# Kernel tuning notes

Measured on AMD Instinct MI355X. Metric: run time of the kernel, lower is better.

The kernel has to match this reference:

```python
import jax, jax.numpy as jnp
import numpy as np

NUM_ENTS = 1000
NUM_RELS = 100
HIDDEN = 200
N_QUERY = 50000
N_HIST = 1000000
ALPHA = 0.5


def setup_inputs() -> dict:
    key = jax.random.key(0)
    ks = jax.random.split(key, 12)
    s = 0.05  # small init for numerical stability (xavier-like scale)
    return {
        "ent_emb": jax.random.normal(ks[0], (NUM_ENTS, HIDDEN), jnp.float32) * s,
        "rel_emb": jax.random.normal(ks[1], (NUM_RELS, HIDDEN), jnp.float32) * s,
        "tim_emb": jax.random.normal(ks[2], (1, HIDDEN), jnp.float32) * s,
        "g_w": jax.random.normal(ks[3], (3 * HIDDEN, HIDDEN), jnp.float32) * s,
        "g_b": jnp.zeros((HIDDEN,), jnp.float32),
        "c_w": jax.random.normal(ks[4], (3 * HIDDEN, HIDDEN), jnp.float32) * s,
        "c_b": jnp.zeros((HIDDEN,), jnp.float32),
        "hist_sub": jax.random.randint(ks[5], (N_HIST,), 0, NUM_ENTS, jnp.int32),
        "hist_rel": jax.random.randint(ks[6], (N_HIST,), 0, NUM_RELS, jnp.int32),
        "hist_obj": jax.random.randint(ks[7], (N_HIST,), 0, NUM_ENTS, jnp.int32),
        "sub": jax.random.randint(ks[8], (N_QUERY,), 0, NUM_ENTS, jnp.int32),
        "rel": jax.random.randint(ks[9], (N_QUERY,), 0, NUM_RELS, jnp.int32),
    }


def reference(ent_emb, rel_emb, tim_emb, g_w, g_b, c_w, c_b,
              hist_sub, hist_rel, hist_obj, sub, rel):
    E = ent_emb.shape[0]
    R = rel_emb.shape[0]
    N = sub.shape[0]
    # Triple-count histogram over all history graphs (fused scatter-add;
    # equivalent to the per-graph python loop vocab[s,r,o] += 1).
    vocab = jnp.zeros((E, R, E), jnp.float32).at[hist_sub, hist_rel, hist_obj].add(1.0)
    # Query features: [N, 3H]
    x = jnp.concatenate(
        [ent_emb[sub], rel_emb[rel], jnp.broadcast_to(tim_emb, (N, tim_emb.shape[1]))],
        axis=1)
    # Generate-mode score distribution
    gscore = jax.nn.softmax(x @ g_w + g_b, axis=1)  # [N, H]
    # Copy-mode mask: 1 where the (sub, rel) pair occurred in history
    mask = (vocab[sub, rel].sum(axis=1, keepdims=True) != 0).astype(x.dtype)  # [N, 1]
    cscore = jax.nn.softmax(jnp.tanh(x @ c_w + c_b) + mask, axis=1)  # [N, H]
    fscore = gscore + ALPHA * (cscore - gscore)
    return jnp.log(fscore)
```

## Files before the change

### kernel.cpp

```cpp
#include <hip/hip_runtime.h>
#include <math.h>

#define HIDDEN 200
#define ROWS_PER_BLOCK 4

__global__ __launch_bounds__(256) void precompute_kernel(
    const float* __restrict__ ent, const float* __restrict__ rel,
    const float* __restrict__ tim,
    const float* __restrict__ g_w, const float* __restrict__ g_b,
    const float* __restrict__ c_w, const float* __restrict__ c_b,
    float* __restrict__ Ag, float* __restrict__ Bg, float* __restrict__ Tg,
    float* __restrict__ Ac, float* __restrict__ Bc, float* __restrict__ Tc) {
  const float* in;
  const float* w;
  const float* bias = nullptr;
  float* out;
  int nrows, k0;
  switch (blockIdx.y) {
    case 0:  in = ent; w = g_w; out = Ag; nrows = 1000; k0 = 0;   break;
    case 1:  in = rel; w = g_w; out = Bg; nrows = 100;  k0 = 200; break;
    case 2:  in = tim; w = g_w; out = Tg; nrows = 1;    k0 = 400; bias = g_b; break;
    case 3:  in = ent; w = c_w; out = Ac; nrows = 1000; k0 = 0;   break;
    case 4:  in = rel; w = c_w; out = Bc; nrows = 100;  k0 = 200; break;
    default: in = tim; w = c_w; out = Tc; nrows = 1;    k0 = 400; bias = c_b; break;
  }
  int row0 = blockIdx.x * ROWS_PER_BLOCK;
  if (row0 >= nrows) return;
  int nr = nrows - row0;
  if (nr > ROWS_PER_BLOCK) nr = ROWS_PER_BLOCK;

  __shared__ float a_lds[ROWS_PER_BLOCK][HIDDEN];
  int c = threadIdx.x;
  if (c < HIDDEN) {
    for (int j = 0; j < nr; ++j) a_lds[j][c] = in[(row0 + j) * HIDDEN + c];
  }
  __syncthreads();
  if (c >= HIDDEN) return;

  float acc[ROWS_PER_BLOCK] = {0.f, 0.f, 0.f, 0.f};
  const float* wp = w + k0 * HIDDEN + c;
  #pragma unroll 4
  for (int k = 0; k < HIDDEN; ++k) {
    float wv = wp[k * HIDDEN];
    #pragma unroll
    for (int j = 0; j < ROWS_PER_BLOCK; ++j) acc[j] += a_lds[j][k] * wv;
  }
  float bv = bias ? bias[c] : 0.f;
  for (int j = 0; j < nr; ++j) out[(row0 + j) * HIDDEN + c] = acc[j] + bv;
}

__global__ __launch_bounds__(256) void query_kernel(
    const float* __restrict__ Ag, const float* __restrict__ Bg,
    const float* __restrict__ Tg, const float* __restrict__ Ac,
    const float* __restrict__ Bc, const float* __restrict__ Tc,
    const int* __restrict__ sub, const int* __restrict__ rel,
    float* __restrict__ out, int N) {
  int gtid = blockIdx.x * blockDim.x + threadIdx.x;
  int q = gtid >> 6;
  int lane = threadIdx.x & 63;
  if (q >= N) return;

  int s = sub[q];
  int r = rel[q];
  bool act = lane < (HIDDEN / 4);

  float lg[4], lc[4];
  float mg = -INFINITY, mc = -INFINITY;
  if (act) {
    float4 a = ((const float4*)(Ag + s * HIDDEN))[lane];
    float4 b = ((const float4*)(Bg + r * HIDDEN))[lane];
    float4 t = ((const float4*)Tg)[lane];
    lg[0] = a.x + b.x + t.x;
    lg[1] = a.y + b.y + t.y;
    lg[2] = a.z + b.z + t.z;
    lg[3] = a.w + b.w + t.w;
    a = ((const float4*)(Ac + s * HIDDEN))[lane];
    b = ((const float4*)(Bc + r * HIDDEN))[lane];
    t = ((const float4*)Tc)[lane];
    lc[0] = tanhf(a.x + b.x + t.x);
    lc[1] = tanhf(a.y + b.y + t.y);
    lc[2] = tanhf(a.z + b.z + t.z);
    lc[3] = tanhf(a.w + b.w + t.w);
    #pragma unroll
    for (int j = 0; j < 4; ++j) {
      mg = fmaxf(mg, lg[j]);
      mc = fmaxf(mc, lc[j]);
    }
  }
  #pragma unroll
  for (int m = 32; m > 0; m >>= 1) {
    mg = fmaxf(mg, __shfl_xor(mg, m));
    mc = fmaxf(mc, __shfl_xor(mc, m));
  }

  float eg[4], ec[4];
  float sg = 0.f, sc = 0.f;
  if (act) {
    #pragma unroll
    for (int j = 0; j < 4; ++j) {
      eg[j] = expf(lg[j] - mg);
      ec[j] = expf(lc[j] - mc);
      sg += eg[j];
      sc += ec[j];
    }
  }
  #pragma unroll
  for (int m = 32; m > 0; m >>= 1) {
    sg += __shfl_xor(sg, m);
    sc += __shfl_xor(sc, m);
  }

  if (act) {
    float ig = 0.5f / sg;
    float ic = 0.5f / sc;
    float4 o;
    o.x = logf(eg[0] * ig + ec[0] * ic);
    o.y = logf(eg[1] * ig + ec[1] * ic);
    o.z = logf(eg[2] * ig + ec[2] * ic);
    o.w = logf(eg[3] * ig + ec[3] * ic);
    ((float4*)(out + q * HIDDEN))[lane] = o;
  }
}

extern "C" void kernel_launch(void* const* d_in, const int* in_sizes, int n_in,
                              void* d_out, int out_size, void* d_ws, size_t ws_size,
                              hipStream_t stream) {
  const float* ent  = (const float*)d_in[0];
  const float* relE = (const float*)d_in[1];
  const float* tim  = (const float*)d_in[2];
  const float* g_w  = (const float*)d_in[3];
  const float* g_b  = (const float*)d_in[4];
  const float* c_w  = (const float*)d_in[5];
  const float* c_b  = (const float*)d_in[6];
  const int* sub = (const int*)d_in[10];
  const int* rel = (const int*)d_in[11];
  float* out = (float*)d_out;
  int N = in_sizes[10];

  float* ws = (float*)d_ws;
  float* Ag = ws;
  float* Ac = ws + 200000;
  float* Bg = ws + 400000;
  float* Bc = ws + 420000;
  float* Tg = ws + 440000;
  float* Tc = ws + 440200;

  dim3 grid1((1000 + ROWS_PER_BLOCK - 1) / ROWS_PER_BLOCK, 6);
  precompute_kernel<<<grid1, 256, 0, stream>>>(ent, relE, tim, g_w, g_b, c_w,
                                               c_b, Ag, Bg, Tg, Ac, Bc, Tc);

  long long threads = (long long)N * 64;
  int blocks = (int)((threads + 255) / 256);
  query_kernel<<<blocks, 256, 0, stream>>>(Ag, Bg, Tg, Ac, Bc, Tc, sub, rel,
                                           out, N);
}
```

Baseline: 131.5 us.

## Fold time term into relation tables, drop softmax max pass, use fast intrinsics

The precompute folds the time-embedding projection and bias into the relation tables, so the query kernel does two gathers per branch instead of three. The query kernel drops the max-reduction pass of both softmaxes, relying on small logits (tanh is bounded and the inputs are small), and uses hardware exp2/rcp/log intrinsics with a clamped exp-based tanh. It also broadcasts indices with readfirstlane, uses nontemporal output stores, and doubles rows per block in the precompute. The trade is numerical robustness: skipping max subtraction can overflow for large generate-mode logits, and the fast intrinsics are less accurate.

```diff
diff --git a/kernel.cpp b/kernel.cpp
--- a/kernel.cpp
+++ b/kernel.cpp
@@ -2,57 +2,73 @@
 #include <math.h>
 
 #define HIDDEN 200
-#define ROWS_PER_BLOCK 4
+#define RPB 8
+
+#define LOG2E 1.4426950408889634f
+#define LN2   0.6931471805599453f
+
+typedef float f32x4 __attribute__((ext_vector_type(4)));
 
 __global__ __launch_bounds__(256) void precompute_kernel(
     const float* __restrict__ ent, const float* __restrict__ rel,
     const float* __restrict__ tim,
     const float* __restrict__ g_w, const float* __restrict__ g_b,
     const float* __restrict__ c_w, const float* __restrict__ c_b,
-    float* __restrict__ Ag, float* __restrict__ Bg, float* __restrict__ Tg,
-    float* __restrict__ Ac, float* __restrict__ Bc, float* __restrict__ Tc) {
+    float* __restrict__ Ag, float* __restrict__ Ac,
+    float* __restrict__ Bg, float* __restrict__ Bc) {
   const float* in;
   const float* w;
   const float* bias = nullptr;
   float* out;
   int nrows, k0;
+  bool fold_tim = false;
   switch (blockIdx.y) {
     case 0:  in = ent; w = g_w; out = Ag; nrows = 1000; k0 = 0;   break;
-    case 1:  in = rel; w = g_w; out = Bg; nrows = 100;  k0 = 200; break;
-    case 2:  in = tim; w = g_w; out = Tg; nrows = 1;    k0 = 400; bias = g_b; break;
-    case 3:  in = ent; w = c_w; out = Ac; nrows = 1000; k0 = 0;   break;
-    case 4:  in = rel; w = c_w; out = Bc; nrows = 100;  k0 = 200; break;
-    default: in = tim; w = c_w; out = Tc; nrows = 1;    k0 = 400; bias = c_b; break;
+    case 1:  in = ent; w = c_w; out = Ac; nrows = 1000; k0 = 0;   break;
+    case 2:  in = rel; w = g_w; out = Bg; nrows = 100;  k0 = 200;
+             fold_tim = true; bias = g_b; break;
+    default: in = rel; w = c_w; out = Bc; nrows = 100;  k0 = 200;
+             fold_tim = true; bias = c_b; break;
   }
-  int row0 = blockIdx.x * ROWS_PER_BLOCK;
+  int row0 = blockIdx.x * RPB;
   if (row0 >= nrows) return;
   int nr = nrows - row0;
-  if (nr > ROWS_PER_BLOCK) nr = ROWS_PER_BLOCK;
+  if (nr > RPB) nr = RPB;
 
-  __shared__ float a_lds[ROWS_PER_BLOCK][HIDDEN];
+  __shared__ float a_lds[RPB][HIDDEN];
+  __shared__ float t_lds[HIDDEN];
   int c = threadIdx.x;
   if (c < HIDDEN) {
     for (int j = 0; j < nr; ++j) a_lds[j][c] = in[(row0 + j) * HIDDEN + c];
+    if (fold_tim) t_lds[c] = tim[c];
   }
   __syncthreads();
   if (c >= HIDDEN) return;
 
-  float acc[ROWS_PER_BLOCK] = {0.f, 0.f, 0.f, 0.f};
+  float acc[RPB];
+  #pragma unroll
+  for (int j = 0; j < RPB; ++j) acc[j] = 0.f;
   const float* wp = w + k0 * HIDDEN + c;
   #pragma unroll 4
   for (int k = 0; k < HIDDEN; ++k) {
     float wv = wp[k * HIDDEN];
     #pragma unroll
-    for (int j = 0; j < ROWS_PER_BLOCK; ++j) acc[j] += a_lds[j][k] * wv;
+    for (int j = 0; j < RPB; ++j) acc[j] += a_lds[j][k] * wv;
   }
-  float bv = bias ? bias[c] : 0.f;
-  for (int j = 0; j < nr; ++j) out[(row0 + j) * HIDDEN + c] = acc[j] + bv;
+  float extra = 0.f;
+  if (fold_tim) {
+    const float* wt = w + 400 * HIDDEN + c;
+    float t = 0.f;
+    #pragma unroll 4
+    for (int k = 0; k < HIDDEN; ++k) t += t_lds[k] * wt[k * HIDDEN];
+    extra = t + bias[c];
+  }
+  for (int j = 0; j < nr; ++j) out[(row0 + j) * HIDDEN + c] = acc[j] + extra;
 }
 
 __global__ __launch_bounds__(256) void query_kernel(
-    const float* __restrict__ Ag, const float* __restrict__ Bg,
-    const float* __restrict__ Tg, const float* __restrict__ Ac,
-    const float* __restrict__ Bc, const float* __restrict__ Tc,
+    const float* __restrict__ Ag, const float* __restrict__ Ac,
+    const float* __restrict__ Bg, const float* __restrict__ Bc,
     const int* __restrict__ sub, const int* __restrict__ rel,
     float* __restrict__ out, int N) {
   int gtid = blockIdx.x * blockDim.x + threadIdx.x;
@@ -60,47 +76,31 @@
   int lane = threadIdx.x & 63;
   if (q >= N) return;
 
-  int s = sub[q];
-  int r = rel[q];
+  int s = __builtin_amdgcn_readfirstlane(sub[q]);
+  int r = __builtin_amdgcn_readfirstlane(rel[q]);
   bool act = lane < (HIDDEN / 4);
-
-  float lg[4], lc[4];
-  float mg = -INFINITY, mc = -INFINITY;
-  if (act) {
-    float4 a = ((const float4*)(Ag + s * HIDDEN))[lane];
-    float4 b = ((const float4*)(Bg + r * HIDDEN))[lane];
-    float4 t = ((const float4*)Tg)[lane];
-    lg[0] = a.x + b.x + t.x;
-    lg[1] = a.y + b.y + t.y;
-    lg[2] = a.z + b.z + t.z;
-    lg[3] = a.w + b.w + t.w;
-    a = ((const float4*)(Ac + s * HIDDEN))[lane];
-    b = ((const float4*)(Bc + r * HIDDEN))[lane];
-    t = ((const float4*)Tc)[lane];
-    lc[0] = tanhf(a.x + b.x + t.x);
-    lc[1] = tanhf(a.y + b.y + t.y);
-    lc[2] = tanhf(a.z + b.z + t.z);
-    lc[3] = tanhf(a.w + b.w + t.w);
-    #pragma unroll
-    for (int j = 0; j < 4; ++j) {
-      mg = fmaxf(mg, lg[j]);
-      mc = fmaxf(mc, lc[j]);
-    }
-  }
-  #pragma unroll
-  for (int m = 32; m > 0; m >>= 1) {
-    mg = fmaxf(mg, __shfl_xor(mg, m));
-    mc = fmaxf(mc, __shfl_xor(mc, m));
-  }
 
   float eg[4], ec[4];
   float sg = 0.f, sc = 0.f;
   if (act) {
+    float4 a = ((const float4*)(Ag + s * HIDDEN))[lane];
+    float4 b = ((const float4*)(Bg + r * HIDDEN))[lane];
+    float lg0 = a.x + b.x, lg1 = a.y + b.y, lg2 = a.z + b.z, lg3 = a.w + b.w;
+    eg[0] = __builtin_amdgcn_exp2f(lg0 * LOG2E);
+    eg[1] = __builtin_amdgcn_exp2f(lg1 * LOG2E);
+    eg[2] = __builtin_amdgcn_exp2f(lg2 * LOG2E);
+    eg[3] = __builtin_amdgcn_exp2f(lg3 * LOG2E);
+    sg = (eg[0] + eg[1]) + (eg[2] + eg[3]);
+
+    a = ((const float4*)(Ac + s * HIDDEN))[lane];
+    b = ((const float4*)(Bc + r * HIDDEN))[lane];
+    float xc[4] = {a.x + b.x, a.y + b.y, a.z + b.z, a.w + b.w};
     #pragma unroll
     for (int j = 0; j < 4; ++j) {
-      eg[j] = expf(lg[j] - mg);
-      ec[j] = expf(lc[j] - mc);
-      sg += eg[j];
+      float x = fminf(fmaxf(xc[j], -10.f), 10.f);
+      float e2 = __builtin_amdgcn_exp2f(x * (2.f * LOG2E));
+      float th = (e2 - 1.f) * __builtin_amdgcn_rcpf(e2 + 1.f);
+      ec[j] = __builtin_amdgcn_exp2f(th * LOG2E);
       sc += ec[j];
     }
   }
@@ -111,14 +111,14 @@
   }
 
   if (act) {
-    float ig = 0.5f / sg;
-    float ic = 0.5f / sc;
-    float4 o;
-    o.x = logf(eg[0] * ig + ec[0] * ic);
-    o.y = logf(eg[1] * ig + ec[1] * ic);
-    o.z = logf(eg[2] * ig + ec[2] * ic);
-    o.w = logf(eg[3] * ig + ec[3] * ic);
-    ((float4*)(out + q * HIDDEN))[lane] = o;
+    float ig = 0.5f * __builtin_amdgcn_rcpf(sg);
+    float ic = 0.5f * __builtin_amdgcn_rcpf(sc);
+    f32x4 o;
+    o.x = __builtin_amdgcn_logf(eg[0] * ig + ec[0] * ic) * LN2;
+    o.y = __builtin_amdgcn_logf(eg[1] * ig + ec[1] * ic) * LN2;
+    o.z = __builtin_amdgcn_logf(eg[2] * ig + ec[2] * ic) * LN2;
+    o.w = __builtin_amdgcn_logf(eg[3] * ig + ec[3] * ic) * LN2;
+    __builtin_nontemporal_store(o, (f32x4*)(out + q * HIDDEN) + lane);
   }
 }
 
@@ -142,15 +142,12 @@
   float* Ac = ws + 200000;
   float* Bg = ws + 400000;
   float* Bc = ws + 420000;
-  float* Tg = ws + 440000;
-  float* Tc = ws + 440200;
 
-  dim3 grid1((1000 + ROWS_PER_BLOCK - 1) / ROWS_PER_BLOCK, 6);
+  dim3 grid1((1000 + RPB - 1) / RPB, 4);
   precompute_kernel<<<grid1, 256, 0, stream>>>(ent, relE, tim, g_w, g_b, c_w,
-                                               c_b, Ag, Bg, Tg, Ac, Bc, Tc);
+                                               c_b, Ag, Ac, Bg, Bc);
 
   long long threads = (long long)N * 64;
   int blocks = (int)((threads + 255) / 256);
-  query_kernel<<<blocks, 256, 0, stream>>>(Ag, Bg, Tg, Ac, Bc, Tc, sub, rel,
-                                           out, N);
+  query_kernel<<<blocks, 256, 0, stream>>>(Ag, Ac, Bg, Bc, sub, rel, out, N);
 }
```

Result: slower. 138.9 us (+5.6%).
